# Performance work log

Hardware: AMD Instinct MI355X
Metric: run time of the kernel (lower is better)

The kernel has to match this reference:

```python
import jax, jax.numpy as jnp
import numpy as np

DIM = 1024
B, L = 4, 4096


def setup_inputs() -> dict:
    key = jax.random.key(0)
    ks = jax.random.split(key, 6)
    s = 1.0 / np.sqrt(DIM)
    x = jax.random.normal(ks[0], (B, L, DIM), dtype=jnp.float32)
    Wk = jax.random.uniform(ks[1], (DIM, DIM), jnp.float32, -s, s)
    bk = jax.random.uniform(ks[2], (DIM,), jnp.float32, -s, s)
    Wv = jax.random.uniform(ks[3], (DIM, DIM), jnp.float32, -s, s)
    bv = jax.random.uniform(ks[4], (DIM,), jnp.float32, -s, s)
    ln_g = jnp.ones((DIM,), jnp.float32)
    ln_b = jnp.zeros((DIM,), jnp.float32)
    Wo = jax.random.uniform(ks[5], (DIM, DIM), jnp.float32, -s, s)
    bo = jnp.zeros((DIM,), jnp.float32)
    return {"x": x, "Wk": Wk, "bk": bk, "Wv": Wv, "bv": bv,
            "ln_g": ln_g, "ln_b": ln_b, "Wo": Wo, "bo": bo}


def reference(x, Wk, bk, Wv, bv, ln_g, ln_b, Wo, bo):
    B_, L_, D = x.shape
    # key/value projections (torch Linear: x @ W.T + b)
    keys = x @ Wk.T + bk
    keys = keys / jnp.maximum(jnp.linalg.norm(keys, axis=-1, keepdims=True), 1e-12)
    values = x @ Wv.T + bv
    # circular convolution via FFT: bind keys with values
    Kf = jnp.fft.rfft(keys, axis=-1)
    Vf = jnp.fft.rfft(values, axis=-1)
    bound = jnp.fft.irfft(Kf * Vf, n=D, axis=-1)
    # cumulative holographic memory over sequence
    memory = jnp.cumsum(bound, axis=1)
    # circular correlation (unbind): conj of key spectrum
    Mf = jnp.fft.rfft(memory, axis=-1)
    retrieved = jnp.fft.irfft(Mf * jnp.conj(Kf), n=D, axis=-1)
    # position-dependent normalization: sqrt(1..L)
    norm = jnp.sqrt(jnp.arange(1, L_ + 1, dtype=x.dtype)).reshape(1, L_, 1)
    r = retrieved / norm
    # LayerNorm (eps=1e-5) + output Linear
    mu = jnp.mean(r, axis=-1, keepdims=True)
    var = jnp.var(r, axis=-1, keepdims=True)
    r_ln = (r - mu) * jax.lax.rsqrt(var + 1e-5) * ln_g + ln_b
    return x + (r_ln @ Wo.T + bo)
```

## Files before the change

### kernel.cpp

```cpp
#include <hip/hip_runtime.h>
#include <math.h>

#define B_SZ 4
#define L_SZ 4096
#define D_SZ 1024
#define M_SZ (B_SZ * L_SZ)
#define NBINS 513
#define CCH   (2 * NBINS)
#define TLEN 8
#define NCH  (L_SZ / TLEN)
#define NG   32

typedef short bf16x8 __attribute__((ext_vector_type(8)));
typedef float f32x4  __attribute__((ext_vector_type(4)));
typedef unsigned short us8 __attribute__((ext_vector_type(8)));

#define AS1 __attribute__((address_space(1)))
#define AS3 __attribute__((address_space(3)))

__device__ inline unsigned short f2bf(float f) {
    unsigned int u = __float_as_uint(f);
    u += 0x7fffu + ((u >> 16) & 1u);
    return (unsigned short)(u >> 16);
}
__device__ inline float bf2f(unsigned short u) {
    return __uint_as_float(((unsigned int)u) << 16);
}

__global__ __launch_bounds__(256) void cast_f32_bf16(
        const float* __restrict__ in, unsigned short* __restrict__ out, int n8) {
    int i = blockIdx.x * 256 + threadIdx.x;
    if (i >= n8) return;
    const float4* p = (const float4*)in + 2 * (size_t)i;
    float4 a = p[0], b = p[1];
    us8 o;
    o[0] = f2bf(a.x); o[1] = f2bf(a.y); o[2] = f2bf(a.z); o[3] = f2bf(a.w);
    o[4] = f2bf(b.x); o[5] = f2bf(b.y); o[6] = f2bf(b.z); o[7] = f2bf(b.w);
    *(us8*)(out + (size_t)i * 8) = o;
}

__global__ __launch_bounds__(256) void cast_w3(
        const float* __restrict__ Wk, const float* __restrict__ Wv,
        const float* __restrict__ Wo,
        unsigned short* __restrict__ WB, unsigned short* __restrict__ Wob, int n8) {
    int i = blockIdx.x * 256 + threadIdx.x;
    if (i >= n8) return;
    const int which = blockIdx.y;
    const float* src = (which == 0) ? Wk : (which == 1) ? Wv : Wo;
    unsigned short* dst = (which == 0) ? WB : (which == 1) ? (WB + D_SZ * D_SZ) : Wob;
    const float4* p = (const float4*)src + 2 * (size_t)i;
    float4 a = p[0], b = p[1];
    us8 o;
    o[0] = f2bf(a.x); o[1] = f2bf(a.y); o[2] = f2bf(a.z); o[3] = f2bf(a.w);
    o[4] = f2bf(b.x); o[5] = f2bf(b.y); o[6] = f2bf(b.z); o[7] = f2bf(b.w);
    *(us8*)(dst + (size_t)i * 8) = o;
}

template<int CNT, bool OBF16>
__global__ __launch_bounds__(512, 4) void gemm_mfma(
        const unsigned short* __restrict__ A, const unsigned short* __restrict__ W,
        const float* __restrict__ bias0, const float* __restrict__ bias1,
        const float* __restrict__ resid,
        void* __restrict__ C0v, void* __restrict__ C1v, int M, int K) {
    __shared__ unsigned short Abuf[3][256 * 32];
    __shared__ unsigned short Bbuf[3][128 * 32];
    const int id   = blockIdx.x;
    const int bx   = (id >> 3) % CNT;
    const int by   = (id & 7) + 8 * (id / (8 * CNT));
    const int tid  = threadIdx.x;
    const int lane = tid & 63;
    const int wid  = tid >> 6;
    const int wr   = wid >> 2;
    const int wc   = wid & 3;
    const int bm   = by * 256;
    const int bn   = bx * 128;

    const int sl = tid >> 3;
    const int sq = (tid & 7) ^ (sl & 7);
    const int srow = 2 * sl + (sq >> 2);
    const int skof = (sq & 3) * 8;
    const unsigned short* Abase = A + (size_t)(bm + srow) * K + skof;
    const unsigned short* Wbase = W + (size_t)(bn + srow) * K + skof;
    const int dstoff = tid * 16;

    auto stage3 = [&](int slot, int kk) {
        __builtin_amdgcn_global_load_lds((const AS1 unsigned int*)(Abase + kk),
            (AS3 unsigned int*)((char*)&Abuf[slot][0] + dstoff), 16, 0, 0);
        __builtin_amdgcn_global_load_lds((const AS1 unsigned int*)(Abase + (size_t)128 * K + kk),
            (AS3 unsigned int*)((char*)&Abuf[slot][128 * 32] + dstoff), 16, 0, 0);
        __builtin_amdgcn_global_load_lds((const AS1 unsigned int*)(Wbase + kk),
            (AS3 unsigned int*)((char*)&Bbuf[slot][0] + dstoff), 16, 0, 0);
    };

    const int fr = lane & 15;
    const int kq = lane >> 4;
    const int rslot = (((((fr & 1) << 2) + kq) ^ ((fr >> 1) & 7)) << 4);
    const int aoff0 = wr * 8192 + (fr >> 1) * 128 + rslot;
    const int boff0 = wc * 2048 + (fr >> 1) * 128 + rslot;

    f32x4 acc[8][2] = {};

    const int nt = K >> 5;
    stage3(0, 0);
    stage3(1, 32);
    asm volatile("s_waitcnt vmcnt(3)" ::: "memory");
    __builtin_amdgcn_s_barrier();
    asm volatile("" ::: "memory");

    int slot = 0, slot2 = 2;
    for (int cur = 0; cur < nt; ++cur) {
        bf16x8 a[8], b[2];
        const char* Ab = (const char*)&Abuf[slot][0];
        const char* Bb = (const char*)&Bbuf[slot][0];
        #pragma unroll
        for (int nf = 0; nf < 2; nf++)
            b[nf] = *(const bf16x8*)(Bb + boff0 + nf * 1024);
        #pragma unroll
        for (int mf = 0; mf < 8; mf++)
            a[mf] = *(const bf16x8*)(Ab + aoff0 + mf * 1024);
        if (cur + 2 < nt) stage3(slot2, (cur + 2) << 5);
        __builtin_amdgcn_s_setprio(1);
        #pragma unroll
        for (int mf = 0; mf < 8; mf++)
            #pragma unroll
            for (int nf = 0; nf < 2; nf++)
                acc[mf][nf] = __builtin_amdgcn_mfma_f32_16x16x32_bf16(
                                  a[mf], b[nf], acc[mf][nf], 0, 0, 0);
        __builtin_amdgcn_s_setprio(0);
        if (cur + 2 < nt) { asm volatile("s_waitcnt vmcnt(3)" ::: "memory"); }
        else              { asm volatile("s_waitcnt vmcnt(0)" ::: "memory"); }
        __builtin_amdgcn_s_barrier();
        asm volatile("" ::: "memory");
        slot  = (slot  == 2) ? 0 : slot  + 1;
        slot2 = (slot2 == 2) ? 0 : slot2 + 1;
    }

    const int col0 = lane & 15;
    const int quad = lane >> 4;
    #pragma unroll
    for (int nf = 0; nf < 2; nf++) {
        const int ng = bn + wc * 32 + nf * 16 + col0;
        const int half = ng >> 10;
        const int n = ng & 1023;
        const float bv = half ? bias1[n] : bias0[n];
        void* Cv = half ? C1v : C0v;
        #pragma unroll
        for (int mf = 0; mf < 8; mf++) {
            #pragma unroll
            for (int r = 0; r < 4; r++) {
                const int m = bm + wr * 128 + mf * 16 + quad * 4 + r;
                float v = acc[mf][nf][r] + bv;
                size_t off = (size_t)m * 1024 + n;
                if constexpr (OBF16) {
                    ((unsigned short*)Cv)[off] = f2bf(v);
                } else {
                    if (resid) v += resid[off];
                    ((float*)Cv)[off] = v;
                }
            }
        }
    }
}

#define SWZ(a) ((a) ^ (((a) >> 4) & 15))

struct cplx { float r, i; };
__device__ inline cplx cmul(cplx a, cplx b) {
    return {a.r * b.r - a.i * b.i, a.r * b.i + a.i * b.r};
}

__device__ inline void r4bfly(cplx v[4], float s) {
    cplx t0 {v[0].r + v[2].r, v[0].i + v[2].i};
    cplx t1 {v[0].r - v[2].r, v[0].i - v[2].i};
    cplx t2 {v[1].r + v[3].r, v[1].i + v[3].i};
    cplx t3 {v[1].r - v[3].r, v[1].i - v[3].i};
    cplx j3 {-s * t3.i, s * t3.r};
    v[0] = {t0.r + t2.r, t0.i + t2.i};
    v[2] = {t0.r - t2.r, t0.i - t2.i};
    v[1] = {t1.r + j3.r, t1.i + j3.i};
    v[3] = {t1.r - j3.r, t1.i - j3.i};
}

template<int SIGN>
__device__ inline void make_w1(cplx w1s[4], int tid) {
    const float s = (float)SIGN;
    #pragma unroll
    for (int q = 1; q <= 3; q++) {
        const int Ls = 1 << (2 * q);
        const float ang = s * 1.57079632679489662f * (float)(tid & (Ls - 1)) / (float)Ls;
        float sn, cs; __sincosf(ang, &sn, &cs);
        w1s[q - 1] = {cs, sn};
    }
    float sn, cs;
    __sincosf(s * 1.57079632679489662f * (float)tid / 256.0f, &sn, &cs);
    w1s[3] = {cs, sn};
}

template<int SIGN>
__device__ inline void fft1024_tw(float2* bA, float2* bB, cplx v[4], int tid,
                                  const cplx w1s[4]) {
    const float s = (float)SIGN;
    r4bfly(v, s);
    {
        const int base = tid << 2;
        #pragma unroll
        for (int e = 0; e < 4; e++)
            bA[SWZ(base + e)] = make_float2(v[e].r, v[e].i);
    }
    __syncthreads();
    float2* cur = bA;
    float2* nxt = bB;
    #pragma unroll
    for (int q = 1; q <= 3; q++) {
        const int Ls = 1 << (2 * q);
        #pragma unroll
        for (int k = 0; k < 4; k++) {
            float2 t = cur[SWZ(tid + (k << 8))];
            v[k] = {t.x, t.y};
        }
        const int d = tid & (Ls - 1);
        cplx w1 = w1s[q - 1];
        cplx w2 = cmul(w1, w1);
        cplx w3 = cmul(w2, w1);
        v[1] = cmul(v[1], w1);
        v[2] = cmul(v[2], w2);
        v[3] = cmul(v[3], w3);
        r4bfly(v, s);
        const int base = ((tid >> (2 * q)) << (2 * q + 2)) + d;
        #pragma unroll
        for (int e = 0; e < 4; e++)
            nxt[SWZ(base + (e << (2 * q)))] = make_float2(v[e].r, v[e].i);
        float2* tmp = cur; cur = nxt; nxt = tmp;
        __syncthreads();
    }
    #pragma unroll
    for (int k = 0; k < 4; k++) {
        float2 t = cur[SWZ(tid + (k << 8))];
        v[k] = {t.x, t.y};
    }
    {
        cplx w1 = w1s[3];
        cplx w2 = cmul(w1, w1);
        cplx w3 = cmul(w2, w1);
        v[1] = cmul(v[1], w1);
        v[2] = cmul(v[2], w2);
        v[3] = cmul(v[3], w3);
        r4bfly(v, s);
    }
}

__global__ __launch_bounds__(256) void bind_cum_kernel(
        unsigned short* __restrict__ KIO, const unsigned short* __restrict__ Vb,
        unsigned short* __restrict__ P, float* __restrict__ totals) {
    __shared__ float2 bA[1024], bB[1024];
    __shared__ float red[4];
    const int blk = blockIdx.x;
    const int tid = threadIdx.x;
    const int wv  = tid >> 6;
    const int ln  = tid & 63;
    const size_t tok0 = (size_t)blk * TLEN;

    cplx w1s[4];
    make_w1<-1>(w1s, tid);

    float r0r = 0.f, r0i = 0.f, r1r = 0.f, r1i = 0.f, r2r = 0.f, r2i = 0.f;

    float kvC[4], vvC[4];
    {
        const unsigned short* krow = KIO + tok0 * D_SZ;
        const unsigned short* vrow = Vb  + tok0 * D_SZ;
        #pragma unroll
        for (int k = 0; k < 4; k++) {
            kvC[k] = bf2f(krow[tid + (k << 8)]);
            vvC[k] = bf2f(vrow[tid + (k << 8)]);
        }
    }

    for (int tk = 0; tk < TLEN; ++tk) {
        const size_t token = tok0 + tk;
        unsigned short* krow = KIO + token * D_SZ;

        float ss = 0.f;
        #pragma unroll
        for (int k = 0; k < 4; k++) ss += kvC[k] * kvC[k];
        #pragma unroll
        for (int m = 1; m < 64; m <<= 1) ss += __shfl_xor(ss, m, 64);
        if (ln == 0) red[wv] = ss;
        __syncthreads();
        const float scale = 1.0f /
            fmaxf(sqrtf(red[0] + red[1] + red[2] + red[3]), 1e-12f);

        cplx z[4];
        #pragma unroll
        for (int k = 0; k < 4; k++) z[k] = {kvC[k] * scale, vvC[k]};

        if (tk + 1 < TLEN) {
            const unsigned short* krowN = KIO + (token + 1) * D_SZ;
            const unsigned short* vrowN = Vb  + (token + 1) * D_SZ;
            #pragma unroll
            for (int k = 0; k < 4; k++) {
                kvC[k] = bf2f(krowN[tid + (k << 8)]);
                vvC[k] = bf2f(vrowN[tid + (k << 8)]);
            }
        }

        fft1024_tw<-1>(bA, bB, z, tid, w1s);

        #pragma unroll
        for (int e = 0; e < 4; e++)
            bA[SWZ(tid + (e << 8))] = make_float2(z[e].r, z[e].i);
        __syncthreads();

        ushort2* Po = (ushort2*)(P + token * CCH);
        auto procbin = [&](int bin, float& rr, float& ri) {
            float2 Zb = bA[SWZ(bin)];
            float2 Zm = bA[SWZ((1024 - bin) & 1023)];
            float ar = 0.5f * (Zb.x + Zm.x);
            float ai = 0.5f * (Zb.y - Zm.y);
            float br = 0.5f * (Zb.y + Zm.y);
            float bi = 0.5f * (Zm.x - Zb.x);
            rr += ar * br - ai * bi;
            ri += ar * bi + ai * br;
            ushort2 pv; pv.x = f2bf(rr); pv.y = f2bf(ri);
            Po[bin] = pv;
            if (bin == 0)        krow[0] = f2bf(ar);
            else if (bin == 512) krow[1] = f2bf(ar);
            else {
                ushort2 kv2; kv2.x = f2bf(ar); kv2.y = f2bf(ai);
                *(ushort2*)(krow + 2 * bin) = kv2;
            }
        };
        procbin(tid,       r0r, r0i);
        procbin(tid + 256, r1r, r1i);
        if (tid == 0) procbin(512, r2r, r2i);
    }

    float* trow = totals + (size_t)blk * CCH;
    trow[2 * tid]             = r0r;  trow[2 * tid + 1]         = r0i;
    trow[2 * (tid + 256)]     = r1r;  trow[2 * (tid + 256) + 1] = r1i;
    if (tid == 0) { trow[1024] = r2r; trow[1025] = r2i; }
}

__global__ __launch_bounds__(256) void scan_s1(
        float* __restrict__ totals, float* __restrict__ gt) {
    const int c = blockIdx.x * 256 + threadIdx.x;
    if (c >= CCH) return;
    const int g = blockIdx.y;
    const int b = blockIdx.z;
    float run = 0.f;
    #pragma unroll
    for (int i = 0; i < 16; i++) {
        size_t idx = ((size_t)(b * NCH + g * 16 + i)) * CCH + c;
        float v = totals[idx];
        totals[idx] = run;
        run += v;
    }
    gt[((size_t)(b * NG + g)) * CCH + c] = run;
}

__global__ __launch_bounds__(256) void scan_s2(float* __restrict__ gt) {
    const int c = blockIdx.x * 256 + threadIdx.x;
    if (c >= CCH) return;
    const int b = blockIdx.y;
    float run = 0.f;
    #pragma unroll
    for (int g = 0; g < NG; g++) {
        size_t idx = ((size_t)(b * NG + g)) * CCH + c;
        float v = gt[idx];
        gt[idx] = run;
        run += v;
    }
}

__global__ __launch_bounds__(256) void unbind4_ln_kernel(
        const unsigned short* __restrict__ P, const float* __restrict__ totals,
        const float* __restrict__ gt, const unsigned short* __restrict__ KF,
        const float* __restrict__ ln_g, const float* __restrict__ ln_b,
        unsigned short* __restrict__ RLNb) {
    __shared__ float2 bA[1024], bB[1024];
    __shared__ float2 offsh[NBINS];
    __shared__ float red[16];
    const int blk = blockIdx.x;
    const int tid = threadIdx.x;
    const int wv  = tid >> 6;
    const int ln  = tid & 63;
    const size_t tok0 = (size_t)blk * TLEN;
    const int bidx  = (int)(tok0 >> 12);
    const int t0    = (int)(tok0 & (L_SZ - 1));
    const int chunk = t0 >> 3;

    {
        const float2* off2 = (const float2*)(totals + (size_t)(bidx * NCH + chunk) * CCH);
        const float2* gof2 = (const float2*)(gt + (size_t)(bidx * NG + (chunk >> 4)) * CCH);
        auto ldo = [&](int bin) {
            float2 o = off2[bin], g = gof2[bin];
            offsh[bin] = make_float2(o.x + g.x, o.y + g.y);
        };
        ldo(tid); ldo(tid + 256);
        if (tid == 0) ldo(512);
    }

    cplx w1s[4];
    make_w1<1>(w1s, tid);

    float gv[4], bev[4];
    #pragma unroll
    for (int e = 0; e < 4; e++) {
        gv[e]  = ln_g[tid + (e << 8)];
        bev[e] = ln_b[tid + (e << 8)];
    }
    __syncthreads();

    for (int p = 0; p < 4; ++p) {
        const size_t ta = tok0 + 2 * p, tb = ta + 1;
        const ushort2* Sa2 = (const ushort2*)(P + ta * CCH);
        const ushort2* Sb2 = (const ushort2*)(P + tb * CCH);
        const unsigned short* Ka = KF + ta * D_SZ;
        const unsigned short* Kb = KF + tb * D_SZ;

        auto zc = [&](int bin, const ushort2* S2, const unsigned short* kf, float2 og) {
            float kr, ki;
            if (bin == 0)        { kr = bf2f(kf[0]); ki = 0.f; }
            else if (bin == 512) { kr = bf2f(kf[1]); ki = 0.f; }
            else {
                ushort2 k2 = *(const ushort2*)(kf + 2 * bin);
                kr = bf2f(k2.x); ki = bf2f(k2.y);
            }
            ushort2 s2 = S2[bin];
            float sr = bf2f(s2.x) + og.x, si = bf2f(s2.y) + og.y;
            return make_float2(sr * kr + si * ki, si * kr - sr * ki);
        };
        auto fill = [&](int bin) {
            float2 og = offsh[bin];
            float2 Za = zc(bin, Sa2, Ka, og);
            float2 Zb = zc(bin, Sb2, Kb, og);
            bA[SWZ(bin)] = make_float2(Za.x - Zb.y, Za.y + Zb.x);
            if (bin != 0 && bin != 512)
                bA[SWZ(1024 - bin)] = make_float2(Za.x + Zb.y, Zb.x - Za.y);
        };
        fill(tid);
        fill(tid + 256);
        if (tid == 0) fill(512);
        __syncthreads();

        cplx z[4];
        #pragma unroll
        for (int k = 0; k < 4; k++) {
            float2 c = bA[SWZ(tid + (k << 8))];
            z[k] = {c.x, c.y};
        }
        __syncthreads();
        fft1024_tw<1>(bA, bB, z, tid, w1s);

        const int t_a = t0 + 2 * p;
        const float sa = (1.0f / 1024.0f) * rsqrtf((float)(t_a + 1));
        const float sb = (1.0f / 1024.0f) * rsqrtf((float)(t_a + 2));
        float ra[4], rb[4];
        float s1a = 0.f, s2a = 0.f, s1b = 0.f, s2b = 0.f;
        #pragma unroll
        for (int e = 0; e < 4; e++) {
            ra[e] = z[e].r * sa;
            rb[e] = z[e].i * sb;
            s1a += ra[e]; s2a += ra[e] * ra[e];
            s1b += rb[e]; s2b += rb[e] * rb[e];
        }
        #pragma unroll
        for (int m = 1; m < 64; m <<= 1) {
            s1a += __shfl_xor(s1a, m, 64);
            s2a += __shfl_xor(s2a, m, 64);
            s1b += __shfl_xor(s1b, m, 64);
            s2b += __shfl_xor(s2b, m, 64);
        }
        if (ln == 0) {
            red[wv] = s1a; red[4 + wv] = s2a; red[8 + wv] = s1b; red[12 + wv] = s2b;
        }
        __syncthreads();
        const float S1a = red[0] + red[1] + red[2] + red[3];
        const float S2a = red[4] + red[5] + red[6] + red[7];
        const float S1b = red[8] + red[9] + red[10] + red[11];
        const float S2b = red[12] + red[13] + red[14] + red[15];
        const float mua = S1a * (1.0f / 1024.0f);
        const float vara = S2a * (1.0f / 1024.0f) - mua * mua;
        const float rsa = rsqrtf(vara + 1e-5f);
        const float mub = S1b * (1.0f / 1024.0f);
        const float varb = S2b * (1.0f / 1024.0f) - mub * mub;
        const float rsb = rsqrtf(varb + 1e-5f);

        unsigned short* outA = RLNb + ta * D_SZ;
        unsigned short* outB = RLNb + tb * D_SZ;
        #pragma unroll
        for (int e = 0; e < 4; e++) {
            const int d = tid + (e << 8);
            outA[d] = f2bf((ra[e] - mua) * rsa * gv[e] + bev[e]);
            outB[d] = f2bf((rb[e] - mub) * rsb * gv[e] + bev[e]);
        }
        __syncthreads();
    }
}

extern "C" void kernel_launch(void* const* d_in, const int* in_sizes, int n_in,
                              void* d_out, int out_size, void* d_ws, size_t ws_size,
                              hipStream_t stream) {
    (void)in_sizes; (void)n_in; (void)out_size; (void)ws_size;
    const float* x    = (const float*)d_in[0];
    const float* Wk   = (const float*)d_in[1];
    const float* bk   = (const float*)d_in[2];
    const float* Wv   = (const float*)d_in[3];
    const float* bv   = (const float*)d_in[4];
    const float* ln_g = (const float*)d_in[5];
    const float* ln_b = (const float*)d_in[6];
    const float* Wo   = (const float*)d_in[7];
    const float* bo   = (const float*)d_in[8];
    float* out = (float*)d_out;

    char* w = (char*)d_ws;
    unsigned short* Kb  = (unsigned short*)w;  w += (size_t)M_SZ * D_SZ * 2;
    unsigned short* Vb  = (unsigned short*)w;  w += (size_t)M_SZ * D_SZ * 2;
    unsigned short* Pb  = (unsigned short*)w;  w += (size_t)M_SZ * CCH * 2;
    unsigned short* xb  = (unsigned short*)w;  w += (size_t)M_SZ * D_SZ * 2;
    unsigned short* WB  = (unsigned short*)w;  w += (size_t)2 * D_SZ * D_SZ * 2;
    unsigned short* Wob = (unsigned short*)w;  w += (size_t)D_SZ * D_SZ * 2;
    unsigned short* RLNb = Vb;
    float* totals = (float*)xb;
    float* gt     = (float*)xb + (size_t)B_SZ * NCH * CCH;

    const int n8x = M_SZ * D_SZ / 8;
    const int n8w = D_SZ * D_SZ / 8;
    cast_f32_bf16<<<n8x / 256, 256, 0, stream>>>(x, xb, n8x);
    dim3 wgrid(n8w / 256, 3);
    cast_w3<<<wgrid, 256, 0, stream>>>(Wk, Wv, Wo, WB, Wob, n8w);

    gemm_mfma<16, true><<<(M_SZ / 256) * 16, 512, 0, stream>>>(
        xb, WB, bk, bv, nullptr, Kb, Vb, M_SZ, D_SZ);

    bind_cum_kernel<<<M_SZ / TLEN, 256, 0, stream>>>(Kb, Vb, Pb, totals);

    dim3 g1((CCH + 255) / 256, NG, B_SZ);
    scan_s1<<<g1, 256, 0, stream>>>(totals, gt);
    dim3 g2((CCH + 255) / 256, B_SZ);
    scan_s2<<<g2, 256, 0, stream>>>(gt);

    unbind4_ln_kernel<<<M_SZ / TLEN, 256, 0, stream>>>(
        Pb, totals, gt, Kb, ln_g, ln_b, RLNb);

    gemm_mfma<8, false><<<(M_SZ / 256) * 8, 512, 0, stream>>>(
        RLNb, Wob, bo, bo, x, out, out, M_SZ, D_SZ);
}
```

Before: 389.7 us.

## Vectorize bind/unbind global accesses with padded spectrum stride and LDS-staged K/V

Pads the per-token spectrum and totals rows to a stride of 1028 so rows stay 8/16-byte aligned. Each thread now handles adjacent bin pairs, so spectrum, key-spectrum and totals reads and writes become ushort4/float4 vector accesses. In the bind kernel the K/V rows are loaded as ushort4, packed and staged through shared memory, which replaces scalar strided loads. This adds a shared buffer and a little extra workspace, and the Nyquist bin moves to a separate path handled by thread 0.

```diff
diff --git a/kernel.cpp b/kernel.cpp
--- a/kernel.cpp
+++ b/kernel.cpp
@@ -6,7 +6,8 @@
 #define D_SZ 1024
 #define M_SZ (B_SZ * L_SZ)
 #define NBINS 513
-#define CCH   (2 * NBINS)
+#define CCH   1026
+#define PSTR  1028
 #define TLEN 8
 #define NCH  (L_SZ / TLEN)
 #define NG   32
@@ -253,6 +254,7 @@
         unsigned short* __restrict__ KIO, const unsigned short* __restrict__ Vb,
         unsigned short* __restrict__ P, float* __restrict__ totals) {
     __shared__ float2 bA[1024], bB[1024];
+    __shared__ unsigned int kvs[1024];
     __shared__ float red[4];
     const int blk = blockIdx.x;
     const int tid = threadIdx.x;
@@ -265,24 +267,31 @@
 
     float r0r = 0.f, r0i = 0.f, r1r = 0.f, r1i = 0.f, r2r = 0.f, r2i = 0.f;
 
-    float kvC[4], vvC[4];
+    ushort4 k4 = *(const ushort4*)(KIO + tok0 * D_SZ + 4 * tid);
+    ushort4 v4 = *(const ushort4*)(Vb  + tok0 * D_SZ + 4 * tid);
     {
-        const unsigned short* krow = KIO + tok0 * D_SZ;
-        const unsigned short* vrow = Vb  + tok0 * D_SZ;
-        #pragma unroll
-        for (int k = 0; k < 4; k++) {
-            kvC[k] = bf2f(krow[tid + (k << 8)]);
-            vvC[k] = bf2f(vrow[tid + (k << 8)]);
-        }
-    }
+        uint4 pk;
+        pk.x = (unsigned int)k4.x | ((unsigned int)v4.x << 16);
+        pk.y = (unsigned int)k4.y | ((unsigned int)v4.y << 16);
+        pk.z = (unsigned int)k4.z | ((unsigned int)v4.z << 16);
+        pk.w = (unsigned int)k4.w | ((unsigned int)v4.w << 16);
+        *(uint4*)&kvs[4 * tid] = pk;
+    }
+    __syncthreads();
 
     for (int tk = 0; tk < TLEN; ++tk) {
         const size_t token = tok0 + tk;
         unsigned short* krow = KIO + token * D_SZ;
 
+        float kvC[4], vvC[4];
         float ss = 0.f;
         #pragma unroll
-        for (int k = 0; k < 4; k++) ss += kvC[k] * kvC[k];
+        for (int k = 0; k < 4; k++) {
+            unsigned int pk = kvs[tid + (k << 8)];
+            kvC[k] = bf2f((unsigned short)(pk & 0xffffu));
+            vvC[k] = bf2f((unsigned short)(pk >> 16));
+            ss += kvC[k] * kvC[k];
+        }
         #pragma unroll
         for (int m = 1; m < 64; m <<= 1) ss += __shfl_xor(ss, m, 64);
         if (ln == 0) red[wv] = ss;
@@ -295,13 +304,8 @@
         for (int k = 0; k < 4; k++) z[k] = {kvC[k] * scale, vvC[k]};
 
         if (tk + 1 < TLEN) {
-            const unsigned short* krowN = KIO + (token + 1) * D_SZ;
-            const unsigned short* vrowN = Vb  + (token + 1) * D_SZ;
-            #pragma unroll
-            for (int k = 0; k < 4; k++) {
-                kvC[k] = bf2f(krowN[tid + (k << 8)]);
-                vvC[k] = bf2f(vrowN[tid + (k << 8)]);
-            }
+            k4 = *(const ushort4*)(KIO + (token + 1) * D_SZ + 4 * tid);
+            v4 = *(const ushort4*)(Vb  + (token + 1) * D_SZ + 4 * tid);
         }
 
         fft1024_tw<-1>(bA, bB, z, tid, w1s);
@@ -309,35 +313,61 @@
         #pragma unroll
         for (int e = 0; e < 4; e++)
             bA[SWZ(tid + (e << 8))] = make_float2(z[e].r, z[e].i);
-        __syncthreads();
-
-        ushort2* Po = (ushort2*)(P + token * CCH);
-        auto procbin = [&](int bin, float& rr, float& ri) {
-            float2 Zb = bA[SWZ(bin)];
-            float2 Zm = bA[SWZ((1024 - bin) & 1023)];
-            float ar = 0.5f * (Zb.x + Zm.x);
-            float ai = 0.5f * (Zb.y - Zm.y);
+        if (tk + 1 < TLEN) {
+            uint4 pk;
+            pk.x = (unsigned int)k4.x | ((unsigned int)v4.x << 16);
+            pk.y = (unsigned int)k4.y | ((unsigned int)v4.y << 16);
+            pk.z = (unsigned int)k4.z | ((unsigned int)v4.z << 16);
+            pk.w = (unsigned int)k4.w | ((unsigned int)v4.w << 16);
+            *(uint4*)&kvs[4 * tid] = pk;
+        }
+        __syncthreads();
+
+        float ar512 = 0.f;
+        if (tid == 0) {
+            float2 Zc = bA[SWZ(512)];
+            r2r += Zc.x * Zc.y;
+            ar512 = Zc.x;
+            ushort2 pv; pv.x = f2bf(r2r); pv.y = f2bf(r2i);
+            *(ushort2*)(P + token * PSTR + 1024) = pv;
+        }
+
+        const int b0 = 2 * tid, b1 = 2 * tid + 1;
+        float ar0, ai0, ar1, ai1;
+        {
+            float2 Zb = bA[SWZ(b0)];
+            float2 Zm = bA[SWZ((1024 - b0) & 1023)];
+            ar0 = 0.5f * (Zb.x + Zm.x);
+            ai0 = 0.5f * (Zb.y - Zm.y);
             float br = 0.5f * (Zb.y + Zm.y);
             float bi = 0.5f * (Zm.x - Zb.x);
-            rr += ar * br - ai * bi;
-            ri += ar * bi + ai * br;
-            ushort2 pv; pv.x = f2bf(rr); pv.y = f2bf(ri);
-            Po[bin] = pv;
-            if (bin == 0)        krow[0] = f2bf(ar);
-            else if (bin == 512) krow[1] = f2bf(ar);
-            else {
-                ushort2 kv2; kv2.x = f2bf(ar); kv2.y = f2bf(ai);
-                *(ushort2*)(krow + 2 * bin) = kv2;
-            }
-        };
-        procbin(tid,       r0r, r0i);
-        procbin(tid + 256, r1r, r1i);
-        if (tid == 0) procbin(512, r2r, r2i);
-    }
-
-    float* trow = totals + (size_t)blk * CCH;
-    trow[2 * tid]             = r0r;  trow[2 * tid + 1]         = r0i;
-    trow[2 * (tid + 256)]     = r1r;  trow[2 * (tid + 256) + 1] = r1i;
+            r0r += ar0 * br - ai0 * bi;
+            r0i += ar0 * bi + ai0 * br;
+        }
+        {
+            float2 Zb = bA[SWZ(b1)];
+            float2 Zm = bA[SWZ(1024 - b1)];
+            ar1 = 0.5f * (Zb.x + Zm.x);
+            ai1 = 0.5f * (Zb.y - Zm.y);
+            float br = 0.5f * (Zb.y + Zm.y);
+            float bi = 0.5f * (Zm.x - Zb.x);
+            r1r += ar1 * br - ai1 * bi;
+            r1i += ar1 * bi + ai1 * br;
+        }
+        ushort4 pw;
+        pw.x = f2bf(r0r); pw.y = f2bf(r0i);
+        pw.z = f2bf(r1r); pw.w = f2bf(r1i);
+        *(ushort4*)(P + token * PSTR + 4 * tid) = pw;
+        ushort4 kfw;
+        kfw.x = f2bf(ar0);
+        kfw.y = (tid == 0) ? f2bf(ar512) : f2bf(ai0);
+        kfw.z = f2bf(ar1); kfw.w = f2bf(ai1);
+        *(ushort4*)(krow + 4 * tid) = kfw;
+    }
+
+    float* trow = totals + (size_t)blk * PSTR;
+    float4 tw; tw.x = r0r; tw.y = r0i; tw.z = r1r; tw.w = r1i;
+    *(float4*)(trow + 4 * tid) = tw;
     if (tid == 0) { trow[1024] = r2r; trow[1025] = r2i; }
 }
 
@@ -350,12 +380,12 @@
     float run = 0.f;
     #pragma unroll
     for (int i = 0; i < 16; i++) {
-        size_t idx = ((size_t)(b * NCH + g * 16 + i)) * CCH + c;
+        size_t idx = ((size_t)(b * NCH + g * 16 + i)) * PSTR + c;
         float v = totals[idx];
         totals[idx] = run;
         run += v;
     }
-    gt[((size_t)(b * NG + g)) * CCH + c] = run;
+    gt[((size_t)(b * NG + g)) * PSTR + c] = run;
 }
 
 __global__ __launch_bounds__(256) void scan_s2(float* __restrict__ gt) {
@@ -365,7 +395,7 @@
     float run = 0.f;
     #pragma unroll
     for (int g = 0; g < NG; g++) {
-        size_t idx = ((size_t)(b * NG + g)) * CCH + c;
+        size_t idx = ((size_t)(b * NG + g)) * PSTR + c;
         float v = gt[idx];
         gt[idx] = run;
         run += v;
@@ -378,7 +408,7 @@
         const float* __restrict__ ln_g, const float* __restrict__ ln_b,
         unsigned short* __restrict__ RLNb) {
     __shared__ float2 bA[1024], bB[1024];
-    __shared__ float2 offsh[NBINS];
+    __shared__ __align__(16) float2 offsh[514];
     __shared__ float red[16];
     const int blk = blockIdx.x;
     const int tid = threadIdx.x;
@@ -390,14 +420,16 @@
     const int chunk = t0 >> 3;
 
     {
-        const float2* off2 = (const float2*)(totals + (size_t)(bidx * NCH + chunk) * CCH);
-        const float2* gof2 = (const float2*)(gt + (size_t)(bidx * NG + (chunk >> 4)) * CCH);
-        auto ldo = [&](int bin) {
-            float2 o = off2[bin], g = gof2[bin];
-            offsh[bin] = make_float2(o.x + g.x, o.y + g.y);
-        };
-        ldo(tid); ldo(tid + 256);
-        if (tid == 0) ldo(512);
+        const float* off2 = totals + (size_t)(bidx * NCH + chunk) * PSTR;
+        const float* gof2 = gt + (size_t)(bidx * NG + (chunk >> 4)) * PSTR;
+        float4 o = *(const float4*)(off2 + 4 * tid);
+        float4 g = *(const float4*)(gof2 + 4 * tid);
+        float4 og; og.x = o.x + g.x; og.y = o.y + g.y;
+        og.z = o.z + g.z; og.w = o.w + g.w;
+        *(float4*)&offsh[2 * tid] = og;
+        if (tid == 0)
+            offsh[512] = make_float2(off2[1024] + gof2[1024],
+                                     off2[1025] + gof2[1025]);
     }
 
     cplx w1s[4];
@@ -411,36 +443,53 @@
     }
     __syncthreads();
 
+    const int b0 = 2 * tid, b1 = 2 * tid + 1;
+
     for (int p = 0; p < 4; ++p) {
         const size_t ta = tok0 + 2 * p, tb = ta + 1;
-        const ushort2* Sa2 = (const ushort2*)(P + ta * CCH);
-        const ushort2* Sb2 = (const ushort2*)(P + tb * CCH);
+        const unsigned short* Pa = P + ta * PSTR;
+        const unsigned short* Pc = P + tb * PSTR;
         const unsigned short* Ka = KF + ta * D_SZ;
-        const unsigned short* Kb = KF + tb * D_SZ;
-
-        auto zc = [&](int bin, const ushort2* S2, const unsigned short* kf, float2 og) {
-            float kr, ki;
-            if (bin == 0)        { kr = bf2f(kf[0]); ki = 0.f; }
-            else if (bin == 512) { kr = bf2f(kf[1]); ki = 0.f; }
-            else {
-                ushort2 k2 = *(const ushort2*)(kf + 2 * bin);
-                kr = bf2f(k2.x); ki = bf2f(k2.y);
-            }
-            ushort2 s2 = S2[bin];
-            float sr = bf2f(s2.x) + og.x, si = bf2f(s2.y) + og.y;
-            return make_float2(sr * kr + si * ki, si * kr - sr * ki);
-        };
-        auto fill = [&](int bin) {
-            float2 og = offsh[bin];
-            float2 Za = zc(bin, Sa2, Ka, og);
-            float2 Zb = zc(bin, Sb2, Kb, og);
-            bA[SWZ(bin)] = make_float2(Za.x - Zb.y, Za.y + Zb.x);
-            if (bin != 0 && bin != 512)
-                bA[SWZ(1024 - bin)] = make_float2(Za.x + Zb.y, Zb.x - Za.y);
-        };
-        fill(tid);
-        fill(tid + 256);
-        if (tid == 0) fill(512);
+        const unsigned short* Kc = KF + tb * D_SZ;
+
+        ushort4 sa = *(const ushort4*)(Pa + 4 * tid);
+        ushort4 sb = *(const ushort4*)(Pc + 4 * tid);
+        ushort4 ka = *(const ushort4*)(Ka + 4 * tid);
+        ushort4 kb = *(const ushort4*)(Kc + 4 * tid);
+        float2 og0 = offsh[b0], og1 = offsh[b1];
+
+        {
+            float ka_r = bf2f(ka.x), ka_i = (tid == 0) ? 0.f : bf2f(ka.y);
+            float kb_r = bf2f(kb.x), kb_i = (tid == 0) ? 0.f : bf2f(kb.y);
+            float sra = bf2f(sa.x) + og0.x, sia = bf2f(sa.y) + og0.y;
+            float srb = bf2f(sb.x) + og0.x, sib = bf2f(sb.y) + og0.y;
+            float Zar = sra * ka_r + sia * ka_i, Zai = sia * ka_r - sra * ka_i;
+            float Zbr = srb * kb_r + sib * kb_i, Zbi = sib * kb_r - srb * kb_i;
+            bA[SWZ(b0)] = make_float2(Zar - Zbi, Zai + Zbr);
+            if (b0 != 0)
+                bA[SWZ(1024 - b0)] = make_float2(Zar + Zbi, Zbr - Zai);
+        }
+        {
+            float ka_r = bf2f(ka.z), ka_i = bf2f(ka.w);
+            float kb_r = bf2f(kb.z), kb_i = bf2f(kb.w);
+            float sra = bf2f(sa.z) + og1.x, sia = bf2f(sa.w) + og1.y;
+            float srb = bf2f(sb.z) + og1.x, sib = bf2f(sb.w) + og1.y;
+            float Zar = sra * ka_r + sia * ka_i, Zai = sia * ka_r - sra * ka_i;
+            float Zbr = srb * kb_r + sib * kb_i, Zbi = sib * kb_r - srb * kb_i;
+            bA[SWZ(b1)] = make_float2(Zar - Zbi, Zai + Zbr);
+            bA[SWZ(1024 - b1)] = make_float2(Zar + Zbi, Zbr - Zai);
+        }
+        if (tid == 0) {
+            ushort2 s5a = *(const ushort2*)(Pa + 1024);
+            ushort2 s5b = *(const ushort2*)(Pc + 1024);
+            float2 og = offsh[512];
+            float kra = bf2f(Ka[1]), krb = bf2f(Kc[1]);
+            float sra = bf2f(s5a.x) + og.x, sia = bf2f(s5a.y) + og.y;
+            float srb = bf2f(s5b.x) + og.x, sib = bf2f(s5b.y) + og.y;
+            float Zar = sra * kra, Zai = sia * kra;
+            float Zbr = srb * krb, Zbi = sib * krb;
+            bA[SWZ(512)] = make_float2(Zar - Zbi, Zai + Zbr);
+        }
         __syncthreads();
 
         cplx z[4];
@@ -453,14 +502,14 @@
         fft1024_tw<1>(bA, bB, z, tid, w1s);
 
         const int t_a = t0 + 2 * p;
-        const float sa = (1.0f / 1024.0f) * rsqrtf((float)(t_a + 1));
-        const float sb = (1.0f / 1024.0f) * rsqrtf((float)(t_a + 2));
+        const float sc_a = (1.0f / 1024.0f) * rsqrtf((float)(t_a + 1));
+        const float sc_b = (1.0f / 1024.0f) * rsqrtf((float)(t_a + 2));
         float ra[4], rb[4];
         float s1a = 0.f, s2a = 0.f, s1b = 0.f, s2b = 0.f;
         #pragma unroll
         for (int e = 0; e < 4; e++) {
-            ra[e] = z[e].r * sa;
-            rb[e] = z[e].i * sb;
+            ra[e] = z[e].r * sc_a;
+            rb[e] = z[e].i * sc_b;
             s1a += ra[e]; s2a += ra[e] * ra[e];
             s1b += rb[e]; s2b += rb[e] * rb[e];
         }
@@ -516,13 +565,13 @@
     char* w = (char*)d_ws;
     unsigned short* Kb  = (unsigned short*)w;  w += (size_t)M_SZ * D_SZ * 2;
     unsigned short* Vb  = (unsigned short*)w;  w += (size_t)M_SZ * D_SZ * 2;
-    unsigned short* Pb  = (unsigned short*)w;  w += (size_t)M_SZ * CCH * 2;
+    unsigned short* Pb  = (unsigned short*)w;  w += (size_t)M_SZ * PSTR * 2;
     unsigned short* xb  = (unsigned short*)w;  w += (size_t)M_SZ * D_SZ * 2;
     unsigned short* WB  = (unsigned short*)w;  w += (size_t)2 * D_SZ * D_SZ * 2;
     unsigned short* Wob = (unsigned short*)w;  w += (size_t)D_SZ * D_SZ * 2;
     unsigned short* RLNb = Vb;
     float* totals = (float*)xb;
-    float* gt     = (float*)xb + (size_t)B_SZ * NCH * CCH;
+    float* gt     = (float*)xb + (size_t)B_SZ * NCH * PSTR;
 
     const int n8x = M_SZ * D_SZ / 8;
     const int n8w = D_SZ * D_SZ / 8;
```

Measured after the change: 379.0 us. -2.7%, faster.
